# Optimization experiments

Measured on AMD Instinct MI355X. Metric: run time of the kernel, lower is better.

## Reference

```python
import jax, jax.numpy as jnp
import numpy as np

SCALE = 20.0
TEMP = 1.0
POW = 0.5
SINK_TAU = 0.3
SINK_ITERS = 30
LAMBDA_LC = 1.0
EPS = 1e-12


def _l2norm(f):
    # F.normalize(f, p=2, dim=channel) * 20 ; f: [B,N,C], normalize over C
    n = jnp.sqrt(jnp.sum(f * f, axis=-1, keepdims=True))
    return f / jnp.maximum(n, EPS) * SCALE


def _sinkhorn(log_alpha, n_iters):
    # log-space Sinkhorn normalization (gumbel_sinkhorn with n_samples=1, no noise)
    def body(la, _):
        la = la - jax.nn.logsumexp(la, axis=2, keepdims=True)  # row normalize
        la = la - jax.nn.logsumexp(la, axis=1, keepdims=True)  # col normalize
        return la, None
    la, _ = jax.lax.scan(body, log_alpha, None, length=n_iters)
    return jnp.exp(la)


def setup_inputs() -> dict:
    key = jax.random.key(0)
    k1, k2 = jax.random.split(key)
    feats = jax.random.normal(k1, (16, 1024, 128), dtype=jnp.float32)
    pc0 = jax.random.normal(k2, (8, 1024, 3), dtype=jnp.float32)
    return {"feats": feats, "pc0": pc0, "epoch": 0}


def reference(feats, pc0, epoch):
    B, N, _ = pc0.shape
    f1 = _l2norm(feats[0::2])                 # [B,N,C]
    f2 = _l2norm(feats[1::2])                 # [B,N,C]
    fa = jnp.roll(f1, -1, axis=0)             # anchor feats1[(b+1)%B]

    corr_1a = jnp.einsum('bnc,bmc->bnm', f1, fa) / TEMP
    smcorr_1a = jax.nn.softmax(corr_1a, axis=2)
    f1_via_fa = jnp.einsum('bnm,bmc->bnc', smcorr_1a, fa)
    corr_1a2 = jnp.einsum('bnc,bmc->bnm', f1_via_fa, f2) / TEMP
    smcorr_1a2 = jax.nn.softmax(corr_1a2, axis=2)

    # Sinkhorn branch is under torch.no_grad()
    sink = jax.lax.stop_gradient(_sinkhorn(corr_1a2 / SINK_TAU, SINK_ITERS))

    # pairwise distance weights (no_grad)
    diff = pc0[:, :, None, :] - pc0[:, None, :, :]            # [B,N,N,3]
    dist = jax.lax.stop_gradient(jnp.sqrt(jnp.sum(diff * diff, axis=-1)) ** POW)

    corr_12 = jnp.einsum('bnc,bmc->bnm', f1, f2)
    smcorr_12 = jax.nn.softmax(corr_12 / TEMP, axis=2)

    L = dist * (smcorr_1a2 + smcorr_12)                       # L = dist*sm1a2 + dist*sm12
    loss = jnp.sum(L) / N                                     # sum over b of L.sum()/N

    eye = jnp.eye(N, dtype=sink.dtype)
    perm_to_I = 3.0 * jnp.sum(jnp.abs(eye[None] - sink)) / N
    Lc = 3.0 * jnp.sum(jnp.abs(sink - smcorr_1a2)) / N

    correct_match = jnp.sum(
        (jnp.argmax(smcorr_1a2, axis=2) == jnp.arange(N)[None, :]).astype(jnp.float32)
    )

    total_loss = loss + LAMBDA_LC * Lc
    Bf = jnp.float32(B)
    return (total_loss / Bf, loss / Bf, Lc / Bf, correct_match / Bf, perm_to_I / Bf)
```

## Files before the change

### kernel.cpp

```cpp
#include <hip/hip_runtime.h>
#include <math.h>

#define NB 8
#define NN 1024
#define NC 128
#define INV_TAU (1.0f/0.3f)
#define LOG2E 1.44269504088896340736f

typedef unsigned short u16;
typedef short bf16x8 __attribute__((ext_vector_type(8)));
typedef float f32x4 __attribute__((ext_vector_type(4)));

__device__ __forceinline__ float wsum(float v){
  #pragma unroll
  for (int o = 32; o > 0; o >>= 1) v += __shfl_xor(v, o, 64);
  return v;
}
__device__ __forceinline__ float wmax(float v){
  #pragma unroll
  for (int o = 32; o > 0; o >>= 1) v = fmaxf(v, __shfl_xor(v, o, 64));
  return v;
}
__device__ __forceinline__ float fexp2(float x){ return __builtin_amdgcn_exp2f(x); }
__device__ __forceinline__ float flog2(float x){ return __builtin_amdgcn_logf(x); }
__device__ __forceinline__ u16 f2bf(float f){
  unsigned u = __float_as_uint(f);
  return (u16)((u + 0x7FFFu + ((u >> 16) & 1u)) >> 16);
}
__device__ __forceinline__ float bf2f(u16 h){ return __uint_as_float((unsigned)h << 16); }

__device__ __forceinline__ void load16(const float* __restrict__ base, int lane, float* o){
  float4 a = *(const float4*)(base + 8 * lane);
  float4 b = *(const float4*)(base + 8 * lane + 4);
  float4 c = *(const float4*)(base + 512 + 8 * lane);
  float4 d = *(const float4*)(base + 512 + 8 * lane + 4);
  o[0]=a.x; o[1]=a.y; o[2]=a.z; o[3]=a.w; o[4]=b.x; o[5]=b.y; o[6]=b.z; o[7]=b.w;
  o[8]=c.x; o[9]=c.y; o[10]=c.z; o[11]=c.w; o[12]=d.x; o[13]=d.y; o[14]=d.z; o[15]=d.w;
}

__global__ void k_init(float* accs, float* P, float* V){
  int i = blockIdx.x * 256 + threadIdx.x;
  if (i < 160) accs[i] = 0.0f;
  P[i] = 0.0f; V[i] = 0.0f;
}

__global__ void k_normalize(const float* __restrict__ feats, float* __restrict__ f1,
                            u16* __restrict__ f1h, u16* __restrict__ f1l,
                            u16* __restrict__ f2h, u16* __restrict__ f2l){
  int vid = blockIdx.x;
  int lane = threadIdx.x;
  const float* src = feats + (size_t)vid * NC;
  float2 x = *(const float2*)(src + lane * 2);
  float s = wsum(x.x * x.x + x.y * x.y);
  float sc = 20.0f / fmaxf(sqrtf(s), 1e-12f);
  int batch = vid >> 10, n = vid & 1023;
  size_t off = ((size_t)(batch >> 1) * NN + n) * NC + 2 * lane;
  float2 y; y.x = x.x * sc; y.y = x.y * sc;
  u16 h0 = f2bf(y.x), h1 = f2bf(y.y);
  u16 l0 = f2bf(y.x - bf2f(h0)), l1 = f2bf(y.y - bf2f(h1));
  unsigned hw = (unsigned)h0 | ((unsigned)h1 << 16);
  unsigned lw = (unsigned)l0 | ((unsigned)l1 << 16);
  if (batch & 1){
    *(unsigned*)(f2h + off) = hw; *(unsigned*)(f2l + off) = lw;
  } else {
    *(float2*)(f1 + off) = y;
    *(unsigned*)(f1h + off) = hw; *(unsigned*)(f1l + off) = lw;
  }
}

__global__ __launch_bounds__(256) void k_gemm_mfma(const u16* __restrict__ Ah,
                                                   const u16* __restrict__ Al,
                                                   const u16* __restrict__ Bh,
                                                   const u16* __restrict__ Bl,
                                                   void* __restrict__ Cm,
                                                   int rollB, int q16){
  const float QS12 = 32766.0f / 400.0f;
  int b = blockIdx.z;
  int n0 = blockIdx.y * 64, m0 = blockIdx.x * 64;
  int tid = threadIdx.x, w = tid >> 6, lane = tid & 63;
  int quad = lane >> 4, l15 = lane & 15;
  int wn = (w >> 1) * 32, wm = (w & 1) * 32;
  size_t abase = (size_t)b * NN * NC;
  size_t bbase = (size_t)((b + rollB) & 7) * NN * NC;
  const u16 *pAh[2], *pAl[2], *pBh[2], *pBl[2];
  #pragma unroll
  for (int i = 0; i < 2; i++){
    size_t ao = abase + (size_t)(n0 + wn + i * 16 + l15) * NC + quad * 8;
    pAh[i] = Ah + ao; pAl[i] = Al + ao;
    size_t bo = bbase + (size_t)(m0 + wm + i * 16 + l15) * NC + quad * 8;
    pBh[i] = Bh + bo; pBl[i] = Bl + bo;
  }
  f32x4 z = {0.0f, 0.0f, 0.0f, 0.0f};
  f32x4 acc[2][2] = {{z, z}, {z, z}};
  #pragma unroll
  for (int k0 = 0; k0 < NC; k0 += 32){
    bf16x8 ah[2], al[2], bh[2], bl[2];
    #pragma unroll
    for (int i = 0; i < 2; i++){
      ah[i] = *(const bf16x8*)(pAh[i] + k0);
      al[i] = *(const bf16x8*)(pAl[i] + k0);
      bh[i] = *(const bf16x8*)(pBh[i] + k0);
      bl[i] = *(const bf16x8*)(pBl[i] + k0);
    }
    #pragma unroll
    for (int i = 0; i < 2; i++)
      #pragma unroll
      for (int j = 0; j < 2; j++){
        acc[i][j] = __builtin_amdgcn_mfma_f32_16x16x32_bf16(ah[i], bh[j], acc[i][j], 0, 0, 0);
        acc[i][j] = __builtin_amdgcn_mfma_f32_16x16x32_bf16(ah[i], bl[j], acc[i][j], 0, 0, 0);
        acc[i][j] = __builtin_amdgcn_mfma_f32_16x16x32_bf16(al[i], bh[j], acc[i][j], 0, 0, 0);
      }
  }
  if (q16){
    short* Cb = (short*)Cm + (size_t)b * NN * NN;
    #pragma unroll
    for (int i = 0; i < 2; i++)
      #pragma unroll
      for (int j = 0; j < 2; j++)
        #pragma unroll
        for (int r = 0; r < 4; r++){
          int n = n0 + wn + i * 16 + quad * 4 + r;
          int m = m0 + wm + j * 16 + l15;
          float q = rintf(fminf(fmaxf(acc[i][j][r] * QS12, -32766.0f), 32766.0f));
          Cb[(size_t)n * NN + m] = (short)(int)q;
        }
  } else {
    float* Cb = (float*)Cm + (size_t)b * NN * NN;
    #pragma unroll
    for (int i = 0; i < 2; i++)
      #pragma unroll
      for (int j = 0; j < 2; j++)
        #pragma unroll
        for (int r = 0; r < 4; r++){
          int n = n0 + wn + i * 16 + quad * 4 + r;
          int m = m0 + wm + j * 16 + l15;
          Cb[(size_t)n * NN + m] = acc[i][j][r];
        }
  }
}

__global__ void k_rowstats(const float* __restrict__ Mb, float* __restrict__ lse){
  int row = blockIdx.x * 4 + (threadIdx.x >> 6);
  int lane = threadIdx.x & 63;
  const float* p = Mb + (size_t)row * NN;
  float x[16]; float mx = -3.402823466e38f;
  #pragma unroll
  for (int k = 0; k < 16; k++){ x[k] = p[lane + 64 * k]; mx = fmaxf(mx, x[k]); }
  mx = wmax(mx);
  float s = 0.0f;
  #pragma unroll
  for (int k = 0; k < 16; k++) s += expf(x[k] - mx);
  s = wsum(s);
  if (lane == 0) lse[row] = mx + logf(s);
}

__global__ void k_rowstats_argmax(const float* __restrict__ Mb, float* __restrict__ lse,
                                  float* __restrict__ accs){
  __shared__ float axs[4];
  int row = blockIdx.x * 4 + (threadIdx.x >> 6);
  int wid = threadIdx.x >> 6;
  int lane = threadIdx.x & 63;
  const float* p = Mb + (size_t)row * NN;
  float x[16]; float mx = -3.402823466e38f; float ax = 0.0f;
  float bm = -3.402823466e38f; int bi = 0;
  #pragma unroll
  for (int k = 0; k < 16; k++){
    x[k] = p[lane + 64 * k];
    mx = fmaxf(mx, x[k]);
    ax = fmaxf(ax, fabsf(x[k]));
    if (x[k] > bm){ bm = x[k]; bi = lane + 64 * k; }
  }
  mx = wmax(mx); ax = wmax(ax);
  #pragma unroll
  for (int o = 32; o > 0; o >>= 1){
    float om = __shfl_xor(bm, o, 64); int oi = __shfl_xor(bi, o, 64);
    if (om > bm || (om == bm && oi < bi)){ bm = om; bi = oi; }
  }
  float s = 0.0f;
  #pragma unroll
  for (int k = 0; k < 16; k++) s += expf(x[k] - mx);
  s = wsum(s);
  if (lane == 0){
    lse[row] = mx + logf(s);
    axs[wid] = ax;
    if (bi == (row & 1023)) atomicAdd(&accs[48 + (blockIdx.x & 15)], 1.0f);
  }
  __syncthreads();
  if (threadIdx.x == 0){
    float a = fmaxf(fmaxf(axs[0], axs[1]), fmaxf(axs[2], axs[3]));
    atomicMax((int*)&accs[64 + (blockIdx.x & 15)], __float_as_int(a));
  }
}

__global__ void k_scale(float* accs){
  if (threadIdx.x == 0){
    float g = 0.0f;
    for (int j = 0; j < 16; j++) g = fmaxf(g, accs[64 + j]);
    accs[80] = (g * INV_TAU * LOG2E) / 32766.0f;
  }
}

__global__ __launch_bounds__(256) void k_fva(const float* __restrict__ Mb,
                                             const float* __restrict__ lse1,
                                             const float* __restrict__ f1,
                                             float* __restrict__ fva){
  __shared__ float Ps[64][36];
  __shared__ float Bs[64][128];
  int b = blockIdx.y;
  int z = blockIdx.z;
  int n0 = blockIdx.x * 32;
  int mbase = z * 512;
  const float* Mrow = Mb + (size_t)(b * NN + n0) * NN + mbase;
  const float* fa = f1 + (size_t)((b + 1) & 7) * NN * NC + (size_t)mbase * NC;
  const float* lseb = lse1 + b * NN + n0;
  float* fvaH = fva + (size_t)z * 1048576;
  int tid = threadIdx.x;
  int ty = tid >> 5, tx = tid & 31;
  float acc[4][4] = {};
  for (int mm = 0; mm < 512; mm += 64){
    #pragma unroll
    for (int i = 0; i < 2; i++){
      int t = tid + 256 * i;
      int r = t >> 4, m4 = t & 15;
      float l = lseb[r];
      float4 v = *(const float4*)(Mrow + (size_t)r * NN + mm + m4 * 4);
      Ps[m4*4+0][r] = expf(v.x - l); Ps[m4*4+1][r] = expf(v.y - l);
      Ps[m4*4+2][r] = expf(v.z - l); Ps[m4*4+3][r] = expf(v.w - l);
    }
    #pragma unroll
    for (int i = 0; i < 8; i++){
      int t = tid + 256 * i;
      int m = t >> 5, c4 = t & 31;
      *(float4*)&Bs[m][c4 * 4] = *(const float4*)(fa + (size_t)(mm + m) * NC + c4 * 4);
    }
    __syncthreads();
    #pragma unroll 8
    for (int m = 0; m < 64; m++){
      float4 a4 = *(const float4*)&Ps[m][ty * 4];
      float4 b4 = *(const float4*)&Bs[m][tx * 4];
      acc[0][0] += a4.x*b4.x; acc[0][1] += a4.x*b4.y; acc[0][2] += a4.x*b4.z; acc[0][3] += a4.x*b4.w;
      acc[1][0] += a4.y*b4.x; acc[1][1] += a4.y*b4.y; acc[1][2] += a4.y*b4.z; acc[1][3] += a4.y*b4.w;
      acc[2][0] += a4.z*b4.x; acc[2][1] += a4.z*b4.y; acc[2][2] += a4.z*b4.z; acc[2][3] += a4.z*b4.w;
      acc[3][0] += a4.w*b4.x; acc[3][1] += a4.w*b4.y; acc[3][2] += a4.w*b4.z; acc[3][3] += a4.w*b4.w;
    }
    __syncthreads();
  }
  #pragma unroll
  for (int i = 0; i < 4; i++){
    float4 o = make_float4(acc[i][0], acc[i][1], acc[i][2], acc[i][3]);
    *(float4*)(fvaH + ((size_t)(b * NN + n0 + ty * 4 + i)) * NC + tx * 4) = o;
  }
}

__global__ __launch_bounds__(256) void k_split(const float* __restrict__ A,
                                               const float* __restrict__ B,
                                               u16* __restrict__ H, u16* __restrict__ L){
  int g = blockIdx.x * 256 + threadIdx.x;
  float4 a = ((const float4*)A)[g];
  float4 b = ((const float4*)B)[g];
  float s[4] = { a.x + b.x, a.y + b.y, a.z + b.z, a.w + b.w };
  u16 h[4], l[4];
  #pragma unroll
  for (int k = 0; k < 4; k++){
    h[k] = f2bf(s[k]);
    l[k] = f2bf(s[k] - bf2f(h[k]));
  }
  uint2 hw, lw;
  hw.x = (unsigned)h[0] | ((unsigned)h[1] << 16); hw.y = (unsigned)h[2] | ((unsigned)h[3] << 16);
  lw.x = (unsigned)l[0] | ((unsigned)l[1] << 16); lw.y = (unsigned)l[2] | ((unsigned)l[3] << 16);
  ((uint2*)H)[g] = hw; ((uint2*)L)[g] = lw;
}

__global__ __launch_bounds__(256) void k_quant_t(const float* __restrict__ Mb,
                                                 const float* __restrict__ accs,
                                                 short* __restrict__ Q,
                                                 short* __restrict__ Qt){
  __shared__ float T[64][68];
  float KQ = (INV_TAU * LOG2E) / accs[80];
  int b = blockIdx.z; int n0 = blockIdx.y * 64, m0 = blockIdx.x * 64;
  const float* src = Mb + (size_t)b * NN * NN;
  int tid = threadIdx.x;
  #pragma unroll
  for (int i = 0; i < 4; i++){
    int t = tid + 256 * i; int r = t >> 4, c4 = t & 15;
    float4 v = *(const float4*)(src + (size_t)(n0 + r) * NN + m0 + c4 * 4);
    float q0 = rintf(v.x * KQ);
    float q1 = rintf(v.y * KQ);
    float q2 = rintf(v.z * KQ);
    float q3 = rintf(v.w * KQ);
    T[r][c4*4+0] = q0; T[r][c4*4+1] = q1; T[r][c4*4+2] = q2; T[r][c4*4+3] = q3;
    int2 w;
    w.x = ((int)q0 & 0xFFFF) | ((int)q1 << 16);
    w.y = ((int)q2 & 0xFFFF) | ((int)q3 << 16);
    *(int2*)(Q + ((size_t)(b * NN + n0 + r) * NN + m0 + c4 * 4)) = w;
  }
  __syncthreads();
  #pragma unroll
  for (int i = 0; i < 4; i++){
    int t = tid + 256 * i; int r = t >> 4, c4 = t & 15;
    float q0 = T[c4*4+0][r], q1 = T[c4*4+1][r], q2 = T[c4*4+2][r], q3 = T[c4*4+3][r];
    int2 w;
    w.x = ((int)q0 & 0xFFFF) | ((int)q1 << 16);
    w.y = ((int)q2 & 0xFFFF) | ((int)q3 << 16);
    *(int2*)(Qt + ((size_t)(b * NN + m0 + r) * NN + n0 + c4 * 4)) = w;
  }
}

__global__ __launch_bounds__(256) void k_pass(const short* __restrict__ Q,
                                              const float* __restrict__ invec,
                                              float* __restrict__ outvec,
                                              const float* __restrict__ accs){
  const float IQ2 = accs[80];
  int tid = threadIdx.x, wid = tid >> 6, lane = tid & 63;
  int row = blockIdx.x * 4 + wid;
  int b = row >> 10;
  float hh[16];
  load16(invec + b * NN, lane, hh);
  const int4* qp = (const int4*)(Q + (size_t)row * NN);
  int4 wa = qp[lane], wb = qp[64 + lane];
  int qq[8] = { wa.x, wa.y, wa.z, wa.w, wb.x, wb.y, wb.z, wb.w };
  float x[16]; float mx = -3.402823466e38f;
  #pragma unroll
  for (int k = 0; k < 8; k++){
    x[2*k]   = fmaf((float)(short)(qq[k]), IQ2, hh[2*k]);
    x[2*k+1] = fmaf((float)(qq[k] >> 16),  IQ2, hh[2*k+1]);
    mx = fmaxf(mx, fmaxf(x[2*k], x[2*k+1]));
  }
  mx = wmax(mx);
  float s = 0.0f;
  #pragma unroll
  for (int k = 0; k < 16; k++) s += fexp2(x[k] - mx);
  s = wsum(s);
  if (lane == 0) outvec[row] = -(mx + flog2(s));
}

__global__ __launch_bounds__(1024) void k_final(const short* __restrict__ Q,
                                                const short* __restrict__ Q12,
                                                const float* __restrict__ lse2,
                                                const float* __restrict__ P2,
                                                const float* __restrict__ V2,
                                                const float* __restrict__ pc0,
                                                float* __restrict__ accs){
  __shared__ float pcx[1152], pcy[1152], pcz[1152];
  __shared__ float partial[3][16];
  const float IQ2 = accs[80];
  const float IQ12_2 = (400.0f / 32766.0f) * LOG2E;
  int tid = threadIdx.x, wid = tid >> 6, lane = tid & 63;
  int row = blockIdx.x * 16 + wid;
  int b = row >> 10, n = row & 1023;
  {
    int m = tid;
    const float* pg = pc0 + (size_t)b * 3072 + 3 * m;
    float px = pg[0], py = pg[1], pz = pg[2];
    int idx = m + (m >> 3);
    pcx[idx] = px; pcy[idx] = py; pcz[idx] = pz;
  }
  __syncthreads();
  const int4* qp  = (const int4*)(Q   + (size_t)row * NN);
  const int4* qp2 = (const int4*)(Q12 + (size_t)row * NN);
  int4 a1 = qp[lane],  b1 = qp[64 + lane];
  int4 a2 = qp2[lane], b2 = qp2[64 + lane];
  int q1[8] = { a1.x, a1.y, a1.z, a1.w, b1.x, b1.y, b1.z, b1.w };
  int q2[8] = { a2.x, a2.y, a2.z, a2.w, b2.x, b2.y, b2.z, b2.w };
  float L[16], c[16];
  float cmx = -3.402823466e38f;
  #pragma unroll
  for (int k = 0; k < 8; k++){
    L[2*k]   = (float)(short)(q1[k]) * IQ2;
    L[2*k+1] = (float)(q1[k] >> 16)  * IQ2;
    c[2*k]   = (float)(short)(q2[k]) * IQ12_2;
    c[2*k+1] = (float)(q2[k] >> 16)  * IQ12_2;
    cmx = fmaxf(cmx, fmaxf(c[2*k], c[2*k+1]));
  }
  cmx = wmax(cmx);
  float cs = 0.0f;
  #pragma unroll
  for (int k = 0; k < 16; k++) cs += fexp2(c[k] - cmx);
  cs = wsum(cs);
  float lse12r = cmx + flog2(cs);
  float vv[16];
  load16(V2 + b * NN, lane, vv);
  int nidx = n + (n >> 3);
  float qx = pcx[nidx], qy = pcy[nidx], qz = pcz[nidx];
  float c1row = -lse2[row] * LOG2E;
  float Prow = P2[row];
  float sl = 0.0f, slc = 0.0f, spi = 0.0f;
  #pragma unroll
  for (int k = 0; k < 16; k++){
    int m = (k < 8) ? (8 * lane + k) : (512 + 8 * lane + k - 8);
    int midx = m + (m >> 3);
    float e1 = fexp2(fmaf(L[k], 0.3f, c1row));
    float sk = fexp2(L[k] + Prow + vv[k]);
    float e2 = fexp2(c[k] - lse12r);
    float dx = qx - pcx[midx], dy = qy - pcy[midx], dz = qz - pcz[midx];
    float d = sqrtf(sqrtf(dx*dx + dy*dy + dz*dz));
    sl  += d * (e1 + e2);
    slc += fabsf(sk - e1);
    spi += fabsf(((m == n) ? 1.0f : 0.0f) - sk);
  }
  sl = wsum(sl); slc = wsum(slc); spi = wsum(spi);
  if (lane == 0){ partial[0][wid] = sl; partial[1][wid] = slc; partial[2][wid] = spi; }
  __syncthreads();
  if (tid < 3){
    float t = 0.0f;
    #pragma unroll
    for (int i = 0; i < 16; i++) t += partial[tid][i];
    atomicAdd(&accs[tid * 16 + (blockIdx.x & 15)], t);
  }
}

__global__ void k_finalize(const float* __restrict__ accs, float* __restrict__ out){
  if (threadIdx.x == 0){
    float sl = 0, slc = 0, spi = 0, scm = 0;
    for (int j = 0; j < 16; j++){
      sl += accs[j]; slc += accs[16 + j]; spi += accs[32 + j]; scm += accs[48 + j];
    }
    float loss = sl / 1024.0f;
    float Lc   = 3.0f * slc / 1024.0f;
    float perm = 3.0f * spi / 1024.0f;
    float total = loss + Lc;
    out[0] = total / 8.0f;
    out[1] = loss / 8.0f;
    out[2] = Lc / 8.0f;
    out[3] = scm / 8.0f;
    out[4] = perm / 8.0f;
  }
}

extern "C" void kernel_launch(void* const* d_in, const int* in_sizes, int n_in,
                              void* d_out, int out_size, void* d_ws, size_t ws_size,
                              hipStream_t stream){
  const float* feats = (const float*)d_in[0];
  const float* pc0   = (const float*)d_in[1];
  float* out = (float*)d_out;

  float* ws   = (float*)d_ws;
  float* f1   = ws;
  u16* f1h    = (u16*)(f1 + 1048576);
  u16* f1l    = f1h + 1048576;
  u16* f2h    = f1l + 1048576;
  u16* f2l    = f2h + 1048576;
  u16* fvh    = f2l + 1048576;
  u16* fvl    = fvh + 1048576;
  float* fva  = (float*)(fvl + 1048576);
  float* M    = fva + 2097152;
  short* Q    = (short*)(M + 8388608);
  short* Qt   = Q + 8388608;
  float* lse1 = (float*)(Qt + 8388608);
  float* lse2 = lse1 + 8192;
  float* P    = lse2 + 8192;
  float* V    = P + 8192;
  float* accs = V + 8192;
  if (ws_size < (size_t)((char*)(accs + 160) - (char*)ws)) return;

  k_init<<<32, 256, 0, stream>>>(accs, P, V);
  k_normalize<<<16384, 64, 0, stream>>>(feats, f1, f1h, f1l, f2h, f2l);
  k_gemm_mfma<<<dim3(16,16,8), 256, 0, stream>>>(f1h, f1l, f1h, f1l, M, 1, 0);
  k_rowstats<<<2048, 256, 0, stream>>>(M, lse1);
  k_fva<<<dim3(32,8,2), 256, 0, stream>>>(M, lse1, f1, fva);
  k_split<<<1024, 256, 0, stream>>>(fva, fva + 1048576, fvh, fvl);
  k_gemm_mfma<<<dim3(16,16,8), 256, 0, stream>>>(fvh, fvl, f2h, f2l, M, 0, 0);
  k_rowstats_argmax<<<2048, 256, 0, stream>>>(M, lse2, accs);
  k_scale<<<1, 64, 0, stream>>>(accs);
  k_quant_t<<<dim3(16,16,8), 256, 0, stream>>>(M, accs, Q, Qt);
  for (int it = 0; it < 30; it++){
    k_pass<<<2048, 256, 0, stream>>>(Q,  V, P, accs);
    k_pass<<<2048, 256, 0, stream>>>(Qt, P, V, accs);
  }
  k_gemm_mfma<<<dim3(16,16,8), 256, 0, stream>>>(f1h, f1l, f2h, f2l, Qt, 0, 1);
  k_final<<<512, 1024, 0, stream>>>(Q, Qt, lse2, P, V, pc0, accs);
  k_finalize<<<1, 64, 0, stream>>>(accs, out);
}
```

Before: 537.4 us.

## Stage GEMM tiles in swizzled LDS with 128x128 block tiles

The split-bf16 MFMA GEMM now loads 128x128 tiles of the hi/lo A and B operands into XOR-swizzled shared memory, and each wave computes a 64x64 sub-tile instead of reading operands straight from global memory into 32x32 wave tiles. This raises operand reuse and cuts redundant global and L2 traffic. The cost is 64 KB of LDS per block, more accumulator registers (lower occupancy), and only 512 blocks per launch. Only the three GEMM launches change; the Sinkhorn passes dominate the rest of the runtime.

Measured after the change: 478.7 us. 10.9% less time.

```diff
diff --git a/kernel.cpp b/kernel.cpp
--- a/kernel.cpp
+++ b/kernel.cpp
@@ -68,55 +68,71 @@
   }
 }
 
-__global__ __launch_bounds__(256) void k_gemm_mfma(const u16* __restrict__ Ah,
-                                                   const u16* __restrict__ Al,
-                                                   const u16* __restrict__ Bh,
-                                                   const u16* __restrict__ Bl,
+__global__ __launch_bounds__(256) void k_gemm_mfma(const u16* __restrict__ Ah_g,
+                                                   const u16* __restrict__ Al_g,
+                                                   const u16* __restrict__ Bh_g,
+                                                   const u16* __restrict__ Bl_g,
                                                    void* __restrict__ Cm,
                                                    int rollB, int q16){
+  __shared__ __align__(16) u16 As_h[128][64];
+  __shared__ __align__(16) u16 As_l[128][64];
+  __shared__ __align__(16) u16 Bs_h[128][64];
+  __shared__ __align__(16) u16 Bs_l[128][64];
   const float QS12 = 32766.0f / 400.0f;
   int b = blockIdx.z;
-  int n0 = blockIdx.y * 64, m0 = blockIdx.x * 64;
+  int m0 = blockIdx.x * 128, n0 = blockIdx.y * 128;
   int tid = threadIdx.x, w = tid >> 6, lane = tid & 63;
   int quad = lane >> 4, l15 = lane & 15;
-  int wn = (w >> 1) * 32, wm = (w & 1) * 32;
+  int wn = (w >> 1) * 64, wm = (w & 1) * 64;
   size_t abase = (size_t)b * NN * NC;
   size_t bbase = (size_t)((b + rollB) & 7) * NN * NC;
-  const u16 *pAh[2], *pAl[2], *pBh[2], *pBl[2];
-  #pragma unroll
-  for (int i = 0; i < 2; i++){
-    size_t ao = abase + (size_t)(n0 + wn + i * 16 + l15) * NC + quad * 8;
-    pAh[i] = Ah + ao; pAl[i] = Al + ao;
-    size_t bo = bbase + (size_t)(m0 + wm + i * 16 + l15) * NC + quad * 8;
-    pBh[i] = Bh + bo; pBl[i] = Bl + bo;
-  }
   f32x4 z = {0.0f, 0.0f, 0.0f, 0.0f};
-  f32x4 acc[2][2] = {{z, z}, {z, z}};
-  #pragma unroll
-  for (int k0 = 0; k0 < NC; k0 += 32){
-    bf16x8 ah[2], al[2], bh[2], bl[2];
-    #pragma unroll
-    for (int i = 0; i < 2; i++){
-      ah[i] = *(const bf16x8*)(pAh[i] + k0);
-      al[i] = *(const bf16x8*)(pAl[i] + k0);
-      bh[i] = *(const bf16x8*)(pBh[i] + k0);
-      bl[i] = *(const bf16x8*)(pBl[i] + k0);
-    }
-    #pragma unroll
-    for (int i = 0; i < 2; i++)
+  f32x4 acc[4][4] = {{z,z,z,z},{z,z,z,z},{z,z,z,z},{z,z,z,z}};
+  for (int kk = 0; kk < NC; kk += 64){
+    #pragma unroll
+    for (int i2 = 0; i2 < 4; i2++){
+      int uidx = tid + 256 * i2;
+      int r = uidx >> 3, u = uidx & 7;
+      int su = ((u ^ (r & 7)) << 3);
+      size_t goA = abase + (size_t)(n0 + r) * NC + kk + u * 8;
+      size_t goB = bbase + (size_t)(m0 + r) * NC + kk + u * 8;
+      *(uint4*)&As_h[r][su] = *(const uint4*)(Ah_g + goA);
+      *(uint4*)&As_l[r][su] = *(const uint4*)(Al_g + goA);
+      *(uint4*)&Bs_h[r][su] = *(const uint4*)(Bh_g + goB);
+      *(uint4*)&Bs_l[r][su] = *(const uint4*)(Bl_g + goB);
+    }
+    __syncthreads();
+    #pragma unroll
+    for (int c = 0; c < 2; c++){
+      bf16x8 ah[4], al[4], bh[4], bl[4];
       #pragma unroll
-      for (int j = 0; j < 2; j++){
-        acc[i][j] = __builtin_amdgcn_mfma_f32_16x16x32_bf16(ah[i], bh[j], acc[i][j], 0, 0, 0);
-        acc[i][j] = __builtin_amdgcn_mfma_f32_16x16x32_bf16(ah[i], bl[j], acc[i][j], 0, 0, 0);
-        acc[i][j] = __builtin_amdgcn_mfma_f32_16x16x32_bf16(al[i], bh[j], acc[i][j], 0, 0, 0);
+      for (int i = 0; i < 4; i++){
+        int rn = wn + i * 16 + l15;
+        int sn = (((c * 4 + quad) ^ (rn & 7)) << 3);
+        ah[i] = *(const bf16x8*)&As_h[rn][sn];
+        al[i] = *(const bf16x8*)&As_l[rn][sn];
+        int rm = wm + i * 16 + l15;
+        int sm = (((c * 4 + quad) ^ (rm & 7)) << 3);
+        bh[i] = *(const bf16x8*)&Bs_h[rm][sm];
+        bl[i] = *(const bf16x8*)&Bs_l[rm][sm];
       }
+      #pragma unroll
+      for (int i = 0; i < 4; i++)
+        #pragma unroll
+        for (int j = 0; j < 4; j++){
+          acc[i][j] = __builtin_amdgcn_mfma_f32_16x16x32_bf16(ah[i], bh[j], acc[i][j], 0, 0, 0);
+          acc[i][j] = __builtin_amdgcn_mfma_f32_16x16x32_bf16(ah[i], bl[j], acc[i][j], 0, 0, 0);
+          acc[i][j] = __builtin_amdgcn_mfma_f32_16x16x32_bf16(al[i], bh[j], acc[i][j], 0, 0, 0);
+        }
+    }
+    __syncthreads();
   }
   if (q16){
     short* Cb = (short*)Cm + (size_t)b * NN * NN;
     #pragma unroll
-    for (int i = 0; i < 2; i++)
+    for (int i = 0; i < 4; i++)
       #pragma unroll
-      for (int j = 0; j < 2; j++)
+      for (int j = 0; j < 4; j++)
         #pragma unroll
         for (int r = 0; r < 4; r++){
           int n = n0 + wn + i * 16 + quad * 4 + r;
@@ -127,9 +143,9 @@
   } else {
     float* Cb = (float*)Cm + (size_t)b * NN * NN;
     #pragma unroll
-    for (int i = 0; i < 2; i++)
+    for (int i = 0; i < 4; i++)
       #pragma unroll
-      for (int j = 0; j < 2; j++)
+      for (int j = 0; j < 4; j++)
         #pragma unroll
         for (int r = 0; r < 4; r++){
           int n = n0 + wn + i * 16 + quad * 4 + r;
@@ -455,11 +471,11 @@
 
   k_init<<<32, 256, 0, stream>>>(accs, P, V);
   k_normalize<<<16384, 64, 0, stream>>>(feats, f1, f1h, f1l, f2h, f2l);
-  k_gemm_mfma<<<dim3(16,16,8), 256, 0, stream>>>(f1h, f1l, f1h, f1l, M, 1, 0);
+  k_gemm_mfma<<<dim3(8,8,8), 256, 0, stream>>>(f1h, f1l, f1h, f1l, M, 1, 0);
   k_rowstats<<<2048, 256, 0, stream>>>(M, lse1);
   k_fva<<<dim3(32,8,2), 256, 0, stream>>>(M, lse1, f1, fva);
   k_split<<<1024, 256, 0, stream>>>(fva, fva + 1048576, fvh, fvl);
-  k_gemm_mfma<<<dim3(16,16,8), 256, 0, stream>>>(fvh, fvl, f2h, f2l, M, 0, 0);
+  k_gemm_mfma<<<dim3(8,8,8), 256, 0, stream>>>(fvh, fvl, f2h, f2l, M, 0, 0);
   k_rowstats_argmax<<<2048, 256, 0, stream>>>(M, lse2, accs);
   k_scale<<<1, 64, 0, stream>>>(accs);
   k_quant_t<<<dim3(16,16,8), 256, 0, stream>>>(M, accs, Q, Qt);
@@ -467,7 +483,7 @@
     k_pass<<<2048, 256, 0, stream>>>(Q,  V, P, accs);
     k_pass<<<2048, 256, 0, stream>>>(Qt, P, V, accs);
   }
-  k_gemm_mfma<<<dim3(16,16,8), 256, 0, stream>>>(f1h, f1l, f2h, f2l, Qt, 0, 1);
+  k_gemm_mfma<<<dim3(8,8,8), 256, 0, stream>>>(f1h, f1l, f2h, f2l, Qt, 0, 1);
   k_final<<<512, 1024, 0, stream>>>(Q, Qt, lse2, P, V, pc0, accs);
   k_finalize<<<1, 64, 0, stream>>>(accs, out);
 }
```
